# Kernel optimization log

Hardware: AMD Instinct MI355X
Metric: run time of the kernel (lower is better)

The kernel has to match this reference:

```python
import jax, jax.numpy as jnp
import numpy as np

FEAT = 39
HID = 1024
SEQ = 254
NCLS = 10
FC1 = 100


def setup_inputs() -> dict:
    key = jax.random.key(0)
    ks = jax.random.split(key, 10)
    B = 128
    x = jax.random.normal(ks[0], (B, SEQ, FEAT), dtype=jnp.float32)
    h0 = jax.random.uniform(ks[1], (B, HID), dtype=jnp.float32)
    s_ih = 1.0 / np.sqrt(HID)
    W_ih = jax.random.uniform(ks[2], (HID, FEAT), jnp.float32, -s_ih, s_ih)
    W_hh = jax.random.uniform(ks[3], (HID, HID), jnp.float32, -s_ih, s_ih)
    b_ih = jax.random.uniform(ks[4], (HID,), jnp.float32, -s_ih, s_ih)
    b_hh = jax.random.uniform(ks[5], (HID,), jnp.float32, -s_ih, s_ih)
    s1 = 1.0 / np.sqrt(SEQ * HID)
    W1 = jax.random.uniform(ks[6], (FC1, SEQ * HID), jnp.float32, -s1, s1)
    b1 = jax.random.uniform(ks[7], (FC1,), jnp.float32, -s1, s1)
    s2 = 1.0 / np.sqrt(FC1)
    W2 = jax.random.uniform(ks[8], (NCLS, FC1), jnp.float32, -s2, s2)
    b2 = jax.random.uniform(ks[9], (NCLS,), jnp.float32, -s2, s2)
    return {"x": x, "h0": h0, "W_ih": W_ih, "W_hh": W_hh, "b_ih": b_ih,
            "b_hh": b_hh, "W1": W1, "b1": b1, "W2": W2, "b2": b2}


def reference(x, h0, W_ih, W_hh, b_ih, b_hh, W1, b1, W2, b2):
    B = x.shape[0]
    # time-major: [SEQ, B, FEAT]
    xt = jnp.transpose(x, (1, 0, 2))
    # precompute input projection for all timesteps: [SEQ, B, HID]
    xproj = jnp.einsum('sbf,hf->sbh', xt, W_ih) + b_ih + b_hh

    def step(h, xp):
        h = jnp.tanh(xp + h @ W_hh.T)
        return h, h

    _, outs = jax.lax.scan(step, h0, xproj)  # outs: [SEQ, B, HID]
    feats = jnp.transpose(outs, (1, 0, 2)).reshape(B, SEQ * HID)
    h1 = jax.nn.relu(feats @ W1.T + b1)
    logits = h1 @ W2.T + b2
    return jax.nn.log_softmax(logits, axis=-1)
```

## Files before the change

kernel.cpp:

```cpp
#include <hip/hip_runtime.h>
#include <hip/hip_bf16.h>
#include <stdint.h>
#include <stddef.h>


typedef unsigned short u16;
typedef unsigned int u32;
typedef __attribute__((ext_vector_type(2))) unsigned int u32x2;
typedef __attribute__((ext_vector_type(4))) float f32x4;
typedef __attribute__((ext_vector_type(4))) unsigned short u16x4;
typedef __attribute__((ext_vector_type(8))) short short8;

#define SEQ   254
#define BATCH 128
#define HID   1024
#define FEAT  39
#define FC1N  100
#define FC1P  112
#define NCLS  10
#define NRING 6
#define SENT  0xAAAAAAAAu

#define OFF_RING  ((size_t)0)
#define OFF_OUTS  (OFF_RING + (size_t)NRING * BATCH * HID * 2)
#define OFF_WHH   (OFF_OUTS + (size_t)SEQ * BATCH * HID * 2)
#define OFF_XP    (OFF_WHH + (size_t)HID * HID * 2)
#define OFF_PART  (OFF_XP + (size_t)SEQ * BATCH * HID * 2)

__device__ inline u16 f2bf(float f){
  union { float f; unsigned u; } v; v.f = f;
  unsigned u = v.u;
  u += 0x7fffu + ((u >> 16) & 1u);
  return (u16)(u >> 16);
}
__device__ inline float bf2f(u16 h){
  union { unsigned u; float f; } v; v.u = ((unsigned)h) << 16;
  return v.f;
}
__device__ inline float fast_tanh(float x){
  float e = __expf(2.0f * x);
  return 1.0f - 2.0f / (e + 1.0f);
}

__device__ inline short8 ld_cohx4(const u16* p){
  short8 r;
  asm volatile("global_load_dwordx4 %0, %1, off sc0 sc1" : "=v"(r) : "v"(p) : "memory");
  return r;
}
__device__ inline void st_cohx2(u16* p, u32x2 v){
  asm volatile("global_store_dwordx2 %0, %1, off sc0 sc1" :: "v"(p), "v"(v) : "memory");
}

__device__ inline bool frag_bad(short8 v){
  union { short8 s; u32 w[4]; } u; u.s = v;
  return (u.w[0] == SENT) | (u.w[1] == SENT) | (u.w[2] == SENT) | (u.w[3] == SENT);
}

__global__ void cvt_f32_bf16_kernel(const float* __restrict__ in, u16* __restrict__ out, int n4){
  int i = blockIdx.x * blockDim.x + threadIdx.x;
  if (i < n4){
    f32x4 v = *(const f32x4*)(in + (size_t)i * 4);
    u16x4 o;
    o[0] = f2bf(v[0]); o[1] = f2bf(v[1]); o[2] = f2bf(v[2]); o[3] = f2bf(v[3]);
    *(u16x4*)(out + (size_t)i * 4) = o;
  }
}

__global__ __launch_bounds__(1024) void xproj_kernel(const float* __restrict__ x,
                                                     const float* __restrict__ W_ih,
                                                     const float* __restrict__ b_ih,
                                                     const float* __restrict__ b_hh,
                                                     u16* __restrict__ xp){
  const int s = blockIdx.x;
  __shared__ float xs[BATCH * (FEAT + 1)];
  for (int i = threadIdx.x; i < BATCH * FEAT; i += 1024){
    int b = i / FEAT, f = i - b * FEAT;
    xs[b * (FEAT + 1) + f] = x[((size_t)b * SEQ + s) * FEAT + f];
  }
  __syncthreads();
  const int h = threadIdx.x;
  float w[FEAT];
  #pragma unroll
  for (int f = 0; f < FEAT; ++f) w[f] = W_ih[h * FEAT + f];
  const float bias = b_ih[h] + b_hh[h];
  for (int b = 0; b < BATCH; ++b){
    float acc = bias;
    #pragma unroll
    for (int f = 0; f < FEAT; ++f) acc += xs[b * (FEAT + 1) + f] * w[f];
    xp[((size_t)s * BATCH + b) * HID + h] = f2bf(acc);
  }
}

__global__ __launch_bounds__(256, 1) void scan_kernel(const u16* __restrict__ whh,
                                                      const u16* __restrict__ xp,
                                                      u16* __restrict__ ring,
                                                      u16* __restrict__ outs){
  __shared__ u16 hsh[2][32][512];

  const int bid  = blockIdx.x;
  const int bgrp = bid & 7;
  const int hgrp = bid >> 3;
  const int wid  = threadIdx.x >> 6;
  const int lane = threadIdx.x & 63;
  const int lr = lane & 15;
  const int lg = lane >> 4;
  const int b_base = bgrp * 16;
  const int h_base = hgrp * 64 + wid * 16;
  const int kk0 = wid * 8;

  short8 breg[32];
  {
    const u16* wp = whh + (size_t)(h_base + lr) * HID + lg * 8;
    #pragma unroll
    for (int kk = 0; kk < 32; ++kk) breg[kk] = *(const short8*)(wp + kk * 32);
  }

  const int b_o = b_base + lr;
  const int h_o = hgrp * 64 + wid * 16 + lg * 4;
  const size_t poll_off = (size_t)(b_base + lr) * HID + lg * 8;
  const size_t st_off   = (size_t)b_o * HID + h_o;

  const u32x2 sent2 = {SENT, SENT};

  u16x4 xv = *(const u16x4*)(xp + (size_t)b_o * HID + h_o);

  for (int s = 0; s < SEQ; ++s){
    st_cohx2(ring + (size_t)((s + 2) % NRING) * (BATCH * HID) + st_off, sent2);

    const u16* pp = ring + (size_t)(s % NRING) * (BATCH * HID) + poll_off;
    short8 f[8];
    u32 bad = 0xFFu;
    while (bad){
      #pragma unroll
      for (int i = 0; i < 8; ++i)
        if (bad & (1u << i)) f[i] = ld_cohx4(pp + (kk0 + i) * 32);
      asm volatile("s_waitcnt vmcnt(0)" ::: "memory");
      __builtin_amdgcn_sched_barrier(0);
      u32 nb = 0;
      #pragma unroll
      for (int i = 0; i < 8; ++i)
        if (bad & (1u << i)) nb |= (__ballot(frag_bad(f[i])) != 0ull) ? (1u << i) : 0u;
      bad = nb;
    }

    u16* wb = &hsh[s & 1][0][0];
    #pragma unroll
    for (int i = 0; i < 8; ++i)
      *(short8*)(wb + (size_t)(kk0 + i) * 512 + lane * 8) = f[i];

    u16x4 xv_next;
    if (s + 1 < SEQ)
      xv_next = *(const u16x4*)(xp + ((size_t)(s + 1) * BATCH + b_o) * HID + h_o);

    __syncthreads();

    f32x4 acc0, acc1 = {0.f, 0.f, 0.f, 0.f};
    acc0[0] = bf2f(xv[0]); acc0[1] = bf2f(xv[1]); acc0[2] = bf2f(xv[2]); acc0[3] = bf2f(xv[3]);
    #pragma unroll
    for (int kk = 0; kk < 32; kk += 2){
      short8 a0 = *(const short8*)(wb + (size_t)kk * 512 + lane * 8);
      short8 a1 = *(const short8*)(wb + (size_t)(kk + 1) * 512 + lane * 8);
      acc0 = __builtin_amdgcn_mfma_f32_16x16x32_bf16(breg[kk],     a0, acc0, 0, 0, 0);
      acc1 = __builtin_amdgcn_mfma_f32_16x16x32_bf16(breg[kk + 1], a1, acc1, 0, 0, 0);
    }

    u32x2 d;
    {
      float v0 = fast_tanh(acc0[0] + acc1[0]);
      float v1 = fast_tanh(acc0[1] + acc1[1]);
      float v2 = fast_tanh(acc0[2] + acc1[2]);
      float v3 = fast_tanh(acc0[3] + acc1[3]);
      d[0] = (u32)f2bf(v0) | ((u32)f2bf(v1) << 16);
      d[1] = (u32)f2bf(v2) | ((u32)f2bf(v3) << 16);
    }
    st_cohx2(ring + (size_t)((s + 1) % NRING) * (BATCH * HID) + st_off, d);
    *(u32x2*)(outs + ((size_t)s * BATCH + b_o) * HID + h_o) = d;

    xv = xv_next;
  }
}

__global__ __launch_bounds__(256) void fc1_kernel(const u16* __restrict__ outs,
                                                  const float* __restrict__ W1,
                                                  float* __restrict__ part){
  const int s = blockIdx.x;
  const int wid  = threadIdx.x >> 6;
  const int lane = threadIdx.x & 63;
  const int lr = lane & 15;
  const int lg = lane >> 4;

  f32x4 acc[2][7];
  const f32x4 zero = {0.f, 0.f, 0.f, 0.f};
  #pragma unroll
  for (int i = 0; i < 2; ++i)
    #pragma unroll
    for (int n = 0; n < 7; ++n) acc[i][n] = zero;

  const u16* pa0 = outs + ((size_t)s * BATCH + wid * 32 + lr) * HID + lg * 8;
  const u16* pa1 = pa0 + 16 * HID;

  for (int kk = 0; kk < 32; ++kk){
    short8 a0 = *(const short8*)(pa0 + kk * 32);
    short8 a1 = *(const short8*)(pa1 + kk * 32);
    #pragma unroll
    for (int nt = 0; nt < 7; ++nt){
      const int j = nt * 16 + lr;
      short8 bf;
      if (j < FC1N){
        const float* wp = W1 + (size_t)j * (SEQ * HID) + (size_t)s * HID + kk * 32 + lg * 8;
        f32x4 w0 = *(const f32x4*)wp;
        f32x4 w1 = *(const f32x4*)(wp + 4);
        #pragma unroll
        for (int r = 0; r < 4; ++r){ bf[r] = (short)f2bf(w0[r]); bf[r + 4] = (short)f2bf(w1[r]); }
      } else {
        #pragma unroll
        for (int r = 0; r < 8; ++r) bf[r] = 0;
      }
      acc[0][nt] = __builtin_amdgcn_mfma_f32_16x16x32_bf16(a0, bf, acc[0][nt], 0, 0, 0);
      acc[1][nt] = __builtin_amdgcn_mfma_f32_16x16x32_bf16(a1, bf, acc[1][nt], 0, 0, 0);
    }
  }

  #pragma unroll
  for (int i = 0; i < 2; ++i)
    #pragma unroll
    for (int nt = 0; nt < 7; ++nt)
      #pragma unroll
      for (int r = 0; r < 4; ++r){
        const int b = wid * 32 + i * 16 + lg * 4 + r;
        const int j = nt * 16 + lr;
        part[((size_t)s * BATCH + b) * FC1P + j] = acc[i][nt][r];
      }
}

__global__ __launch_bounds__(128) void reduce_kernel(const float* __restrict__ part,
                                                     const float* __restrict__ b1,
                                                     const float* __restrict__ W2,
                                                     const float* __restrict__ b2,
                                                     float* __restrict__ out){
  const int b = blockIdx.x;
  const int j = threadIdx.x;
  __shared__ float h1[FC1N];
  __shared__ float lgt[NCLS];

  if (j < FC1P){
    const float* p = part + (size_t)b * FC1P + j;
    float acc = 0.f;
    #pragma unroll 4
    for (int s = 0; s < SEQ; ++s) acc += p[(size_t)s * BATCH * FC1P];
    if (j < FC1N) h1[j] = fmaxf(acc + b1[j], 0.f);
  }
  __syncthreads();
  if (j < NCLS){
    float v = b2[j];
    for (int q = 0; q < FC1N; ++q) v += h1[q] * W2[j * FC1N + q];
    lgt[j] = v;
  }
  __syncthreads();
  if (j < NCLS){
    float m = lgt[0];
    #pragma unroll
    for (int q = 1; q < NCLS; ++q) m = fmaxf(m, lgt[q]);
    float sum = 0.f;
    #pragma unroll
    for (int q = 0; q < NCLS; ++q) sum += __expf(lgt[q] - m);
    out[b * NCLS + j] = lgt[j] - (m + __logf(sum));
  }
}

extern "C" void kernel_launch(void* const* d_in, const int* in_sizes, int n_in,
                              void* d_out, int out_size, void* d_ws, size_t ws_size,
                              hipStream_t stream){
  (void)in_sizes; (void)n_in; (void)out_size; (void)ws_size;
  const float* x   = (const float*)d_in[0];
  const float* h0  = (const float*)d_in[1];
  const float* Wih = (const float*)d_in[2];
  const float* Whh = (const float*)d_in[3];
  const float* bih = (const float*)d_in[4];
  const float* bhh = (const float*)d_in[5];
  const float* W1  = (const float*)d_in[6];
  const float* b1  = (const float*)d_in[7];
  const float* W2  = (const float*)d_in[8];
  const float* b2  = (const float*)d_in[9];
  float* out = (float*)d_out;

  char* ws = (char*)d_ws;
  u16*  ring = (u16*)(ws + OFF_RING);
  u16*  outs = (u16*)(ws + OFF_OUTS);
  u16*  whh  = (u16*)(ws + OFF_WHH);
  u16*  xp   = (u16*)(ws + OFF_XP);
  float* part = (float*)(ws + OFF_PART);

  hipMemsetAsync(ring + (size_t)BATCH * HID, 0xAA, (size_t)(NRING - 1) * BATCH * HID * 2, stream);
  cvt_f32_bf16_kernel<<<1024, 256, 0, stream>>>(Whh, whh, (HID * HID) / 4);
  cvt_f32_bf16_kernel<<<128, 256, 0, stream>>>(h0, ring, (BATCH * HID) / 4);
  xproj_kernel<<<SEQ, 1024, 0, stream>>>(x, Wih, bih, bhh, xp);
  scan_kernel<<<128, 256, 0, stream>>>(whh, xp, ring, outs);
  fc1_kernel<<<SEQ, 256, 0, stream>>>(outs, W1, part);
  reduce_kernel<<<BATCH, 128, 0, stream>>>(part, b1, W2, b2, out);
}
```

Baseline: 1.513 ms.

## Have each wave poll the full hidden state directly, dropping LDS staging and block barrier

Each wave now loads all 32 K-fragments of the previous hidden state straight from the global ring into registers and polls them itself. Before, each of the four waves loaded 8 fragments, shared them through LDS and waited at a block barrier. This removes the LDS round trip and the __syncthreads from the serial per-step critical path. The cost is four times more redundant global/L2 traffic per block, more VGPR pressure from holding 32 fragments, and a retry that re-reads all fragments. The sentinel write moves to three slots ahead, and the xproj load is now issued after polling rather than prefetched.

```diff
diff --git a/kernel.cpp b/kernel.cpp
--- a/kernel.cpp
+++ b/kernel.cpp
@@ -42,18 +42,19 @@
   return 1.0f - 2.0f / (e + 1.0f);
 }
 
-__device__ inline short8 ld_cohx4(const u16* p){
+__device__ inline short8 ld_cohx4_off(const u16* p, int imm_bytes){
   short8 r;
-  asm volatile("global_load_dwordx4 %0, %1, off sc0 sc1" : "=v"(r) : "v"(p) : "memory");
+  asm volatile("global_load_dwordx4 %0, %1, off offset:%2 sc0 sc1"
+               : "=v"(r) : "v"(p), "i"(imm_bytes) : "memory");
   return r;
 }
 __device__ inline void st_cohx2(u16* p, u32x2 v){
   asm volatile("global_store_dwordx2 %0, %1, off sc0 sc1" :: "v"(p), "v"(v) : "memory");
 }
 
-__device__ inline bool frag_bad(short8 v){
+__device__ inline u32 frag_bad(short8 v){
   union { short8 s; u32 w[4]; } u; u.s = v;
-  return (u.w[0] == SENT) | (u.w[1] == SENT) | (u.w[2] == SENT) | (u.w[3] == SENT);
+  return (u32)((u.w[0] == SENT) | (u.w[1] == SENT) | (u.w[2] == SENT) | (u.w[3] == SENT));
 }
 
 __global__ void cvt_f32_bf16_kernel(const float* __restrict__ in, u16* __restrict__ out, int n4){
@@ -95,8 +96,6 @@
                                                       const u16* __restrict__ xp,
                                                       u16* __restrict__ ring,
                                                       u16* __restrict__ outs){
-  __shared__ u16 hsh[2][32][512];
-
   const int bid  = blockIdx.x;
   const int bgrp = bid & 7;
   const int hgrp = bid >> 3;
@@ -106,7 +105,6 @@
   const int lg = lane >> 4;
   const int b_base = bgrp * 16;
   const int h_base = hgrp * 64 + wid * 16;
-  const int kk0 = wid * 8;
 
   short8 breg[32];
   {
@@ -116,67 +114,49 @@
   }
 
   const int b_o = b_base + lr;
-  const int h_o = hgrp * 64 + wid * 16 + lg * 4;
+  const int h_o = h_base + lg * 4;
   const size_t poll_off = (size_t)(b_base + lr) * HID + lg * 8;
   const size_t st_off   = (size_t)b_o * HID + h_o;
 
   const u32x2 sent2 = {SENT, SENT};
 
-  u16x4 xv = *(const u16x4*)(xp + (size_t)b_o * HID + h_o);
-
   for (int s = 0; s < SEQ; ++s){
-    st_cohx2(ring + (size_t)((s + 2) % NRING) * (BATCH * HID) + st_off, sent2);
-
-    const u16* pp = ring + (size_t)(s % NRING) * (BATCH * HID) + poll_off;
-    short8 f[8];
-    u32 bad = 0xFFu;
-    while (bad){
+    st_cohx2(ring + (size_t)((s + 3) % NRING) * (BATCH * HID) + st_off, sent2);
+
+    const u16* pa = ring + (size_t)(s % NRING) * (BATCH * HID) + poll_off;
+    short8 a[32];
+    for (;;){
       #pragma unroll
-      for (int i = 0; i < 8; ++i)
-        if (bad & (1u << i)) f[i] = ld_cohx4(pp + (kk0 + i) * 32);
+      for (int kk = 0; kk < 32; ++kk) a[kk] = ld_cohx4_off(pa, kk * 64);
       asm volatile("s_waitcnt vmcnt(0)" ::: "memory");
       __builtin_amdgcn_sched_barrier(0);
-      u32 nb = 0;
+      u32 any = 0;
       #pragma unroll
-      for (int i = 0; i < 8; ++i)
-        if (bad & (1u << i)) nb |= (__ballot(frag_bad(f[i])) != 0ull) ? (1u << i) : 0u;
-      bad = nb;
-    }
-
-    u16* wb = &hsh[s & 1][0][0];
-    #pragma unroll
-    for (int i = 0; i < 8; ++i)
-      *(short8*)(wb + (size_t)(kk0 + i) * 512 + lane * 8) = f[i];
-
-    u16x4 xv_next;
-    if (s + 1 < SEQ)
-      xv_next = *(const u16x4*)(xp + ((size_t)(s + 1) * BATCH + b_o) * HID + h_o);
-
-    __syncthreads();
-
-    f32x4 acc0, acc1 = {0.f, 0.f, 0.f, 0.f};
-    acc0[0] = bf2f(xv[0]); acc0[1] = bf2f(xv[1]); acc0[2] = bf2f(xv[2]); acc0[3] = bf2f(xv[3]);
+      for (int kk = 0; kk < 32; ++kk) any |= frag_bad(a[kk]);
+      if (__ballot(any) == 0ull) break;
+    }
+    __builtin_amdgcn_sched_barrier(0);
+
+    u16x4 xv = *(const u16x4*)(xp + ((size_t)s * BATCH + b_o) * HID + h_o);
+
+    f32x4 acc0 = {0.f, 0.f, 0.f, 0.f}, acc1 = {0.f, 0.f, 0.f, 0.f};
     #pragma unroll
     for (int kk = 0; kk < 32; kk += 2){
-      short8 a0 = *(const short8*)(wb + (size_t)kk * 512 + lane * 8);
-      short8 a1 = *(const short8*)(wb + (size_t)(kk + 1) * 512 + lane * 8);
-      acc0 = __builtin_amdgcn_mfma_f32_16x16x32_bf16(breg[kk],     a0, acc0, 0, 0, 0);
-      acc1 = __builtin_amdgcn_mfma_f32_16x16x32_bf16(breg[kk + 1], a1, acc1, 0, 0, 0);
+      acc0 = __builtin_amdgcn_mfma_f32_16x16x32_bf16(breg[kk],     a[kk],     acc0, 0, 0, 0);
+      acc1 = __builtin_amdgcn_mfma_f32_16x16x32_bf16(breg[kk + 1], a[kk + 1], acc1, 0, 0, 0);
     }
 
     u32x2 d;
     {
-      float v0 = fast_tanh(acc0[0] + acc1[0]);
-      float v1 = fast_tanh(acc0[1] + acc1[1]);
-      float v2 = fast_tanh(acc0[2] + acc1[2]);
-      float v3 = fast_tanh(acc0[3] + acc1[3]);
+      float v0 = fast_tanh(acc0[0] + acc1[0] + bf2f(xv[0]));
+      float v1 = fast_tanh(acc0[1] + acc1[1] + bf2f(xv[1]));
+      float v2 = fast_tanh(acc0[2] + acc1[2] + bf2f(xv[2]));
+      float v3 = fast_tanh(acc0[3] + acc1[3] + bf2f(xv[3]));
       d[0] = (u32)f2bf(v0) | ((u32)f2bf(v1) << 16);
       d[1] = (u32)f2bf(v2) | ((u32)f2bf(v3) << 16);
     }
     st_cohx2(ring + (size_t)((s + 1) % NRING) * (BATCH * HID) + st_off, d);
     *(u32x2*)(outs + ((size_t)s * BATCH + b_o) * HID + h_o) = d;
-
-    xv = xv_next;
   }
 }
 
```

After: 2.916 ms. 1.93x slower.
